# Kernel optimization log

Measured on AMD Instinct MI355X. Metric: run time of the kernel, lower is better.

Reference implementation:

```python
import jax, jax.numpy as jnp
import numpy as np

BN_EPS = 1e-5


def euclid_fc(x, w):
    """-1/2 * ||x_b - w_:,j||^2 for each (batch b, output j).
    x: [B, in], w: [in, out] -> [B, out].
    Uses the algebraic identity ||x-w||^2 = ||x||^2 - 2 x.w + ||w||^2,
    mathematically identical to the broadcast subtract-square-sum.
    """
    x_sq = jnp.sum(x * x, axis=-1, keepdims=True)      # [B, 1]
    w_sq = jnp.sum(w * w, axis=0)                       # [out]
    xw = x @ w                                          # [B, out]
    return -0.5 * (x_sq - 2.0 * xw + w_sq)


def batchnorm_train(x, gamma, beta):
    # BatchNorm1d in training mode: batch mean, biased variance, eps=1e-5
    mean = jnp.mean(x, axis=0)
    var = jnp.var(x, axis=0)  # biased, matches torch normalization stats
    return gamma * (x - mean) / jnp.sqrt(var + BN_EPS) + beta


def setup_inputs() -> dict:
    key = jax.random.key(0)
    ks = jax.random.split(key, 6)
    B, N_in, N2, N_bot, N_out = 1024, 784, 392, 8, 784
    X = jax.random.uniform(ks[0], (B, N_in), dtype=jnp.float32)
    W1 = jax.random.normal(ks[1], (N_in, N2), dtype=jnp.float32)
    W2 = jax.random.normal(ks[2], (N2, N_bot), dtype=jnp.float32)
    W3 = jax.random.normal(ks[3], (N_bot, N2), dtype=jnp.float32)
    W4 = jax.random.normal(ks[4], (N2, N_out), dtype=jnp.float32)
    return {
        "X": X,
        "W1": W1, "g1": jnp.ones((N2,), jnp.float32), "b1": jnp.zeros((N2,), jnp.float32),
        "W2": W2, "g2": jnp.ones((N_bot,), jnp.float32), "b2": jnp.zeros((N_bot,), jnp.float32),
        "W3": W3, "g3": jnp.ones((N2,), jnp.float32), "b3": jnp.zeros((N2,), jnp.float32),
        "W4": W4, "g4": jnp.ones((N_out,), jnp.float32), "b4": jnp.zeros((N_out,), jnp.float32),
    }


def reference(X, W1, g1, b1, W2, g2, b2, W3, g3, b3, W4, g4, b4):
    h = jax.nn.relu(batchnorm_train(euclid_fc(X, W1), g1, b1))
    h = jax.nn.relu(batchnorm_train(euclid_fc(h, W2), g2, b2))
    h = jax.nn.relu(batchnorm_train(euclid_fc(h, W3), g3, b3))
    out = jax.nn.sigmoid(batchnorm_train(euclid_fc(h, W4), g4, b4))
    return out
```

## Files before the change

kernel.cpp:

```cpp
#include <hip/hip_runtime.h>
#include <hip/hip_bf16.h>
#include <math.h>

#define BATCH 1024
#define BM 64
#define BN 64
#define BK 64
#define LDK 72
#define NRB 16

typedef __attribute__((ext_vector_type(8))) short bf16x8;
typedef __attribute__((ext_vector_type(8))) ushort ushort8;
typedef __attribute__((ext_vector_type(4))) float f32x4;

static __device__ __forceinline__ ushort f2bf(float f) {
    union { float f; unsigned u; } v; v.f = f;
    unsigned r = (v.u + 0x7fffu + ((v.u >> 16) & 1u)) >> 16;
    return (ushort)r;
}
static __device__ __forceinline__ float bf2f(ushort u) {
    union { unsigned u; float f; } v; v.u = ((unsigned)u) << 16;
    return v.f;
}

struct GemmSh {
    ushort As[2][BM][LDK];
    ushort Bs[2][BN][LDK];
    float bred[4 * BN];
    float xsq_s[BM], wsq_s[BN];
    float cs[2][BN], cq[2][BN];
};
struct Sh {
    union { float ptile[64][65]; GemmSh g; } u;
    float scaleK[784], shiftK[784];
};

static __device__ __forceinline__ void finalize_stats(
    const float2* __restrict__ stats_in, const float* __restrict__ gamma,
    const float* __restrict__ beta, int K, Sh& sh, int tid)
{
    for (int k = tid; k < K; k += 256) {
        const f32x4* p4 = (const f32x4*)(stats_in + (size_t)k * NRB);
        double s = 0.0, q = 0.0;
        #pragma unroll
        for (int i = 0; i < NRB / 2; ++i) {
            f32x4 v = p4[i];
            s += (double)v[0]; q += (double)v[1];
            s += (double)v[2]; q += (double)v[3];
        }
        double mean = s * (1.0 / BATCH);
        double var = q * (1.0 / BATCH) - mean * mean;
        float inv = (float)(1.0 / sqrt(var + 1e-5));
        float sc = gamma[k] * inv;
        sh.scaleK[k] = sc;
        sh.shiftK[k] = beta[k] - (float)mean * sc;
    }
    __syncthreads();
}

template <int NORM, int BSRC>
static __device__ void gemm_body(
    const float* __restrict__ A, const float* __restrict__ Bw32, const ushort* __restrict__ Wt,
    const float2* __restrict__ stats_in, const float* __restrict__ gamma, const float* __restrict__ beta,
    float* __restrict__ Z, float2* __restrict__ stats_out,
    int K, int N, int cx, int rb, Sh& sh, int tid)
{
    GemmSh& G = sh.u.g;
    const int lane = tid & 63;
    const int wv = tid >> 6;
    const int wr = wv >> 1, wc = wv & 1;
    const int row0 = rb * BM, col0 = cx * BN;
    const int ar = tid >> 3;
    const int ak0 = (tid & 7) * 8;
    const int bn = tid & 63;
    const int bk0 = (tid >> 6) * 16;
    const int fr = lane & 15;
    const int fg = lane >> 4;

    if (NORM) finalize_stats(stats_in, gamma, beta, K, sh, tid);

    f32x4 acc[2][2] = {};
    float asq[2] = {0.f, 0.f};
    float bsq = 0.f;
    float areg[2][8];
    float breg[16];
    ushort8 bh[2];
    const int ntiles = (K + BK - 1) / BK;

    auto load_tile = [&](int t) {
        const int kbase = t * BK;
        const int gc = col0 + bn;
        if (kbase + BK <= K) {
            #pragma unroll
            for (int l = 0; l < 2; ++l) {
                const float* p = A + (size_t)(row0 + ar + 32 * l) * K + kbase + ak0;
                f32x4 v0 = *(const f32x4*)p;
                f32x4 v1 = *(const f32x4*)(p + 4);
                #pragma unroll
                for (int j = 0; j < 4; ++j) { areg[l][j] = v0[j]; areg[l][4 + j] = v1[j]; }
                if (NORM) {
                    #pragma unroll
                    for (int j = 0; j < 8; ++j)
                        areg[l][j] = fmaxf(areg[l][j] * sh.scaleK[kbase + ak0 + j] + sh.shiftK[kbase + ak0 + j], 0.f);
                }
            }
            if (BSRC == 0) {
                #pragma unroll
                for (int i = 0; i < 16; ++i)
                    breg[i] = (gc < N) ? Bw32[(size_t)(kbase + bk0 + i) * N + gc] : 0.f;
            } else {
                if (gc < N) {
                    const ushort* q = Wt + (size_t)gc * K + kbase + bk0;
                    bh[0] = *(const ushort8*)q;
                    bh[1] = *(const ushort8*)(q + 8);
                } else {
                    bh[0] = (ushort8)0; bh[1] = (ushort8)0;
                }
            }
        } else {
            #pragma unroll
            for (int l = 0; l < 2; ++l)
                #pragma unroll
                for (int j = 0; j < 8; ++j) {
                    int gk = kbase + ak0 + j;
                    float x = 0.f;
                    if (gk < K) {
                        x = A[(size_t)(row0 + ar + 32 * l) * K + gk];
                        if (NORM) x = fmaxf(x * sh.scaleK[gk] + sh.shiftK[gk], 0.f);
                    }
                    areg[l][j] = x;
                }
            if (BSRC == 0) {
                #pragma unroll
                for (int i = 0; i < 16; ++i) {
                    int gk = kbase + bk0 + i;
                    breg[i] = (gk < K && gc < N) ? Bw32[(size_t)gk * N + gc] : 0.f;
                }
            } else {
                #pragma unroll
                for (int i = 0; i < 16; ++i) {
                    int gk = kbase + bk0 + i;
                    ushort u = (gk < K && gc < N) ? Wt[(size_t)gc * K + gk] : (ushort)0;
                    bh[i >> 3][i & 7] = u;
                }
            }
        }
    };

    auto store_tile = [&](int buf) {
        #pragma unroll
        for (int l = 0; l < 2; ++l) {
            ushort8 h;
            #pragma unroll
            for (int j = 0; j < 8; ++j) {
                h[j] = f2bf(areg[l][j]);
                asq[l] += areg[l][j] * areg[l][j];
            }
            *(ushort8*)&G.As[buf][ar + 32 * l][ak0] = h;
        }
        if (BSRC == 0) {
            ushort8 e0, e1;
            #pragma unroll
            for (int i = 0; i < 8; ++i) {
                e0[i] = f2bf(breg[i]);      bsq += breg[i] * breg[i];
                e1[i] = f2bf(breg[8 + i]);  bsq += breg[8 + i] * breg[8 + i];
            }
            *(ushort8*)&G.Bs[buf][bn][bk0] = e0;
            *(ushort8*)&G.Bs[buf][bn][bk0 + 8] = e1;
        } else {
            #pragma unroll
            for (int i = 0; i < 8; ++i) {
                float f0 = bf2f(bh[0][i]); bsq += f0 * f0;
                float f1 = bf2f(bh[1][i]); bsq += f1 * f1;
            }
            *(ushort8*)&G.Bs[buf][bn][bk0] = bh[0];
            *(ushort8*)&G.Bs[buf][bn][bk0 + 8] = bh[1];
        }
    };

    auto compute = [&](int buf) {
        bf16x8 af[2][2], bfr[2][2];
        #pragma unroll
        for (int m = 0; m < 2; ++m)
            #pragma unroll
            for (int kk = 0; kk < 2; ++kk)
                af[m][kk] = *(const bf16x8*)&G.As[buf][wr * 32 + m * 16 + fr][kk * 32 + fg * 8];
        #pragma unroll
        for (int n = 0; n < 2; ++n)
            #pragma unroll
            for (int kk = 0; kk < 2; ++kk)
                bfr[n][kk] = *(const bf16x8*)&G.Bs[buf][wc * 32 + n * 16 + fr][kk * 32 + fg * 8];
        #pragma unroll
        for (int m = 0; m < 2; ++m)
            #pragma unroll
            for (int n = 0; n < 2; ++n)
                #pragma unroll
                for (int kk = 0; kk < 2; ++kk)
                    acc[m][n] = __builtin_amdgcn_mfma_f32_16x16x32_bf16(af[m][kk], bfr[n][kk], acc[m][n], 0, 0, 0);
    };

    load_tile(0);
    store_tile(0);
    __syncthreads();
    for (int t = 0; t < ntiles; ++t) {
        if (t + 1 < ntiles) load_tile(t + 1);
        compute(t & 1);
        if (t + 1 < ntiles) store_tile((t + 1) & 1);
        __syncthreads();
    }

    #pragma unroll
    for (int l = 0; l < 2; ++l) {
        float s = asq[l];
        s += __shfl_xor(s, 1, 64);
        s += __shfl_xor(s, 2, 64);
        s += __shfl_xor(s, 4, 64);
        if ((tid & 7) == 0) G.xsq_s[ar + 32 * l] = s;
    }
    G.bred[(tid >> 6) * BN + bn] = bsq;
    __syncthreads();
    if (tid < BN) G.wsq_s[tid] = G.bred[0*BN+tid] + G.bred[1*BN+tid] + G.bred[2*BN+tid] + G.bred[3*BN+tid];
    __syncthreads();

    #pragma unroll
    for (int n = 0; n < 2; ++n) {
        const int c64 = wc * 32 + n * 16 + fr;
        const int c = col0 + c64;
        const float wsq = G.wsq_s[c64];
        float ps = 0.f, pq = 0.f;
        #pragma unroll
        for (int m = 0; m < 2; ++m) {
            #pragma unroll
            for (int j = 0; j < 4; ++j) {
                const int rl = wr * 32 + m * 16 + fg * 4 + j;
                float zv = acc[m][n][j] - 0.5f * (G.xsq_s[rl] + wsq);
                ps += zv; pq += zv * zv;
                if (c < N) Z[(size_t)(row0 + rl) * N + c] = zv;
            }
        }
        ps += __shfl_xor(ps, 16, 64); ps += __shfl_xor(ps, 32, 64);
        pq += __shfl_xor(pq, 16, 64); pq += __shfl_xor(pq, 32, 64);
        if (fg == 0) { G.cs[wr][c64] = ps; G.cq[wr][c64] = pq; }
    }
    __syncthreads();
    if (tid < BN) {
        int c = col0 + tid;
        if (c < N)
            stats_out[(size_t)c * NRB + rb] = make_float2(G.cs[0][tid] + G.cs[1][tid],
                                                          G.cq[0][tid] + G.cq[1][tid]);
    }
}

__global__ __launch_bounds__(256) void l1_kernel(
    const float* __restrict__ X, const float* __restrict__ W1,
    const float* __restrict__ W2, const float* __restrict__ W3, const float* __restrict__ W4,
    ushort* __restrict__ Wt2, ushort* __restrict__ Wt3, ushort* __restrict__ Wt4,
    float* __restrict__ z1, float2* __restrict__ st1)
{
    __shared__ Sh sh;
    const int tid = threadIdx.x;
    const int bid = blockIdx.x;

    if (bid < 112) {
        gemm_body<0, 0>(X, W1, nullptr, nullptr, nullptr, nullptr,
                        z1, st1, 784, 392, bid / 16, bid % 16, sh, tid);
        return;
    }
    for (int t = bid - 112; t < 105; t += 32) {
        const float* W; ushort* Wt; int K, N, kt, nt;
        if (t < 7)       { W = W2; Wt = Wt2; K = 392; N = 8;   kt = t;     nt = 0; }
        else if (t < 14) { W = W3; Wt = Wt3; K = 8;   N = 392; kt = 0;     nt = t - 7; }
        else             { int r = t - 14; W = W4; Wt = Wt4; K = 392; N = 784; kt = r % 7; nt = r / 7; }
        const int k0 = kt * 64, n0 = nt * 64;
        #pragma unroll
        for (int it = 0; it < 16; ++it) {
            int e = it * 256 + tid;
            int kk = e >> 6, nn = e & 63;
            int gk = k0 + kk, gn = n0 + nn;
            sh.u.ptile[kk][nn] = (gk < K && gn < N) ? W[(size_t)gk * N + gn] : 0.f;
        }
        __syncthreads();
        #pragma unroll
        for (int it = 0; it < 16; ++it) {
            int e = it * 256 + tid;
            int nn = e >> 6, kk = e & 63;
            int gk = k0 + kk, gn = n0 + nn;
            if (gk < K && gn < N) Wt[(size_t)gn * K + gk] = f2bf(sh.u.ptile[kk][nn]);
        }
        __syncthreads();
    }
}

__global__ __launch_bounds__(256) void gemm_norm_kernel(
    const float* __restrict__ A, const ushort* __restrict__ Wt,
    const float2* __restrict__ stats_in, const float* __restrict__ gamma, const float* __restrict__ beta,
    float* __restrict__ Z, float2* __restrict__ stats_out, int K, int N)
{
    __shared__ Sh sh;
    gemm_body<1, 1>(A, nullptr, Wt, stats_in, gamma, beta, Z, stats_out,
                    K, N, blockIdx.x / 16, blockIdx.x % 16, sh, threadIdx.x);
}

__global__ __launch_bounds__(256) void bn_sigmoid_inplace(
    float* __restrict__ Zout, const float2* __restrict__ stats,
    const float* __restrict__ gamma, const float* __restrict__ beta)
{
    const int N = 784;
    const int c0 = blockIdx.x * 16;
    const int r0 = blockIdx.y * 128;
    const int tid = threadIdx.x;
    __shared__ float sc16[16], sh16[16];

    if (tid < 16) {
        int k = c0 + tid;
        const f32x4* p4 = (const f32x4*)(stats + (size_t)k * NRB);
        double s = 0.0, q = 0.0;
        #pragma unroll
        for (int i = 0; i < NRB / 2; ++i) {
            f32x4 v = p4[i];
            s += (double)v[0]; q += (double)v[1];
            s += (double)v[2]; q += (double)v[3];
        }
        double mean = s * (1.0 / BATCH);
        double var = q * (1.0 / BATCH) - mean * mean;
        float inv = (float)(1.0 / sqrt(var + 1e-5));
        float scv = gamma[k] * inv;
        sc16[tid] = scv;
        sh16[tid] = beta[k] - (float)mean * scv;
    }
    __syncthreads();

    const int row = r0 + (tid & 127);
    const int ch = tid >> 7;
    float* p = Zout + (size_t)row * N + c0 + ch * 8;
    f32x4 v0 = *(f32x4*)p;
    f32x4 v1 = *(f32x4*)(p + 4);
    #pragma unroll
    for (int j = 0; j < 4; ++j) {
        float y0 = v0[j] * sc16[ch * 8 + j] + sh16[ch * 8 + j];
        v0[j] = 1.f / (1.f + expf(-y0));
        float y1 = v1[j] * sc16[ch * 8 + 4 + j] + sh16[ch * 8 + 4 + j];
        v1[j] = 1.f / (1.f + expf(-y1));
    }
    *(f32x4*)p = v0;
    *(f32x4*)(p + 4) = v1;
}

extern "C" void kernel_launch(void* const* d_in, const int* in_sizes, int n_in,
                              void* d_out, int out_size, void* d_ws, size_t ws_size,
                              hipStream_t stream) {
    const float* X  = (const float*)d_in[0];
    const float* W1 = (const float*)d_in[1];
    const float* g1 = (const float*)d_in[2];
    const float* b1 = (const float*)d_in[3];
    const float* W2 = (const float*)d_in[4];
    const float* g2 = (const float*)d_in[5];
    const float* b2 = (const float*)d_in[6];
    const float* W3 = (const float*)d_in[7];
    const float* g3 = (const float*)d_in[8];
    const float* b3 = (const float*)d_in[9];
    const float* W4 = (const float*)d_in[10];
    const float* g4 = (const float*)d_in[11];
    const float* b4 = (const float*)d_in[12];

    float* ws = (float*)d_ws;
    float*  z1  = ws;
    float*  z2  = z1 + 1024 * 392;
    float*  z3  = z2 + 1024 * 8;
    float2* st1 = (float2*)(z3 + 1024 * 392);
    float2* st2 = st1 + 392 * NRB;
    float2* st3 = st2 + 8 * NRB;
    float2* st4 = st3 + 392 * NRB;
    ushort* Wt2 = (ushort*)(st4 + 784 * NRB);
    ushort* Wt3 = Wt2 + 8 * 392;
    ushort* Wt4 = Wt3 + 392 * 8;
    float* outp = (float*)d_out;

    l1_kernel<<<144, 256, 0, stream>>>(X, W1, W2, W3, W4, Wt2, Wt3, Wt4, z1, st1);
    gemm_norm_kernel<<<16, 256, 0, stream>>>(z1, Wt2, st1, g1, b1, z2, st2, 392, 8);
    gemm_norm_kernel<<<112, 256, 0, stream>>>(z2, Wt3, st2, g2, b2, z3, st3, 8, 392);
    gemm_norm_kernel<<<208, 256, 0, stream>>>(z3, Wt4, st3, g3, b3, outp, st4, 392, 784);
    bn_sigmoid_inplace<<<dim3(49, 8), 256, 0, stream>>>(outp, st4, g4, b4);
}
```

Before: 67.29 us.

## Fuse layers 1-3 into one cooperative kernel with atomic flag gating

Merges the layer-1 GEMM, W4 transpose, layer-2 GEMM and the layer-3 FC/BN into a single cooperative launch. Dependent blocks spin on global atomic counters instead of waiting at kernel boundaries. Layer 3 (K=8) is now computed directly in registers with per-block full-batch BN statistics and writes a bf16 activation for layer 4, which reads bf16 A directly. The goal is to remove three kernel launches and the intermediate fp32 traffic, at the cost of spin-wait blocks, redundant BN2 statistics in each layer-3 block, and an added memset.

```diff
diff --git a/kernel.cpp b/kernel.cpp
--- a/kernel.cpp
+++ b/kernel.cpp
@@ -35,6 +35,20 @@
     float scaleK[784], shiftK[784];
 };
 
+static __device__ __forceinline__ void gate_signal(unsigned* f) {
+    __threadfence();
+    __syncthreads();
+    if (threadIdx.x == 0)
+        __hip_atomic_fetch_add(f, 1u, __ATOMIC_RELAXED, __HIP_MEMORY_SCOPE_AGENT);
+}
+static __device__ __forceinline__ void gate_wait(const unsigned* f, unsigned tgt) {
+    if (threadIdx.x == 0)
+        while (__hip_atomic_load(f, __ATOMIC_RELAXED, __HIP_MEMORY_SCOPE_AGENT) < tgt)
+            __builtin_amdgcn_s_sleep(2);
+    __syncthreads();
+    __threadfence();
+}
+
 static __device__ __forceinline__ void finalize_stats(
     const float2* __restrict__ stats_in, const float* __restrict__ gamma,
     const float* __restrict__ beta, int K, Sh& sh, int tid)
@@ -58,9 +72,10 @@
     __syncthreads();
 }
 
-template <int NORM, int BSRC>
+template <int NORM, int BSRC, int ASRC, int STATS>
 static __device__ void gemm_body(
-    const float* __restrict__ A, const float* __restrict__ Bw32, const ushort* __restrict__ Wt,
+    const float* __restrict__ A32, const ushort* __restrict__ A16,
+    const float* __restrict__ Bw32, const ushort* __restrict__ Wt,
     const float2* __restrict__ stats_in, const float* __restrict__ gamma, const float* __restrict__ beta,
     float* __restrict__ Z, float2* __restrict__ stats_out,
     int K, int N, int cx, int rb, Sh& sh, int tid)
@@ -83,6 +98,7 @@
     float asq[2] = {0.f, 0.f};
     float bsq = 0.f;
     float areg[2][8];
+    ushort8 ah[2];
     float breg[16];
     ushort8 bh[2];
     const int ntiles = (K + BK - 1) / BK;
@@ -93,15 +109,19 @@
         if (kbase + BK <= K) {
             #pragma unroll
             for (int l = 0; l < 2; ++l) {
-                const float* p = A + (size_t)(row0 + ar + 32 * l) * K + kbase + ak0;
-                f32x4 v0 = *(const f32x4*)p;
-                f32x4 v1 = *(const f32x4*)(p + 4);
-                #pragma unroll
-                for (int j = 0; j < 4; ++j) { areg[l][j] = v0[j]; areg[l][4 + j] = v1[j]; }
-                if (NORM) {
+                if (ASRC == 0) {
+                    const float* p = A32 + (size_t)(row0 + ar + 32 * l) * K + kbase + ak0;
+                    f32x4 v0 = *(const f32x4*)p;
+                    f32x4 v1 = *(const f32x4*)(p + 4);
                     #pragma unroll
-                    for (int j = 0; j < 8; ++j)
-                        areg[l][j] = fmaxf(areg[l][j] * sh.scaleK[kbase + ak0 + j] + sh.shiftK[kbase + ak0 + j], 0.f);
+                    for (int j = 0; j < 4; ++j) { areg[l][j] = v0[j]; areg[l][4 + j] = v1[j]; }
+                    if (NORM) {
+                        #pragma unroll
+                        for (int j = 0; j < 8; ++j)
+                            areg[l][j] = fmaxf(areg[l][j] * sh.scaleK[kbase + ak0 + j] + sh.shiftK[kbase + ak0 + j], 0.f);
+                    }
+                } else {
+                    ah[l] = *(const ushort8*)(A16 + (size_t)(row0 + ar + 32 * l) * K + kbase + ak0);
                 }
             }
             if (BSRC == 0) {
@@ -123,12 +143,16 @@
                 #pragma unroll
                 for (int j = 0; j < 8; ++j) {
                     int gk = kbase + ak0 + j;
-                    float x = 0.f;
-                    if (gk < K) {
-                        x = A[(size_t)(row0 + ar + 32 * l) * K + gk];
-                        if (NORM) x = fmaxf(x * sh.scaleK[gk] + sh.shiftK[gk], 0.f);
+                    if (ASRC == 0) {
+                        float x = 0.f;
+                        if (gk < K) {
+                            x = A32[(size_t)(row0 + ar + 32 * l) * K + gk];
+                            if (NORM) x = fmaxf(x * sh.scaleK[gk] + sh.shiftK[gk], 0.f);
+                        }
+                        areg[l][j] = x;
+                    } else {
+                        ah[l][j] = (gk < K) ? A16[(size_t)(row0 + ar + 32 * l) * K + gk] : (ushort)0;
                     }
-                    areg[l][j] = x;
                 }
             if (BSRC == 0) {
                 #pragma unroll
@@ -140,8 +164,7 @@
                 #pragma unroll
                 for (int i = 0; i < 16; ++i) {
                     int gk = kbase + bk0 + i;
-                    ushort u = (gk < K && gc < N) ? Wt[(size_t)gc * K + gk] : (ushort)0;
-                    bh[i >> 3][i & 7] = u;
+                    bh[i >> 3][i & 7] = (gk < K && gc < N) ? Wt[(size_t)gc * K + gk] : (ushort)0;
                 }
             }
         }
@@ -150,13 +173,22 @@
     auto store_tile = [&](int buf) {
         #pragma unroll
         for (int l = 0; l < 2; ++l) {
-            ushort8 h;
-            #pragma unroll
-            for (int j = 0; j < 8; ++j) {
-                h[j] = f2bf(areg[l][j]);
-                asq[l] += areg[l][j] * areg[l][j];
-            }
-            *(ushort8*)&G.As[buf][ar + 32 * l][ak0] = h;
+            if (ASRC == 0) {
+                ushort8 h;
+                #pragma unroll
+                for (int j = 0; j < 8; ++j) {
+                    h[j] = f2bf(areg[l][j]);
+                    asq[l] += areg[l][j] * areg[l][j];
+                }
+                *(ushort8*)&G.As[buf][ar + 32 * l][ak0] = h;
+            } else {
+                #pragma unroll
+                for (int j = 0; j < 8; ++j) {
+                    float x = bf2f(ah[l][j]);
+                    asq[l] += x * x;
+                }
+                *(ushort8*)&G.As[buf][ar + 32 * l][ak0] = ah[l];
+            }
         }
         if (BSRC == 0) {
             ushort8 e0, e1;
@@ -234,71 +266,188 @@
             for (int j = 0; j < 4; ++j) {
                 const int rl = wr * 32 + m * 16 + fg * 4 + j;
                 float zv = acc[m][n][j] - 0.5f * (G.xsq_s[rl] + wsq);
-                ps += zv; pq += zv * zv;
+                if (STATS) { ps += zv; pq += zv * zv; }
                 if (c < N) Z[(size_t)(row0 + rl) * N + c] = zv;
             }
         }
-        ps += __shfl_xor(ps, 16, 64); ps += __shfl_xor(ps, 32, 64);
-        pq += __shfl_xor(pq, 16, 64); pq += __shfl_xor(pq, 32, 64);
-        if (fg == 0) { G.cs[wr][c64] = ps; G.cq[wr][c64] = pq; }
-    }
-    __syncthreads();
-    if (tid < BN) {
-        int c = col0 + tid;
-        if (c < N)
-            stats_out[(size_t)c * NRB + rb] = make_float2(G.cs[0][tid] + G.cs[1][tid],
-                                                          G.cq[0][tid] + G.cq[1][tid]);
-    }
-}
-
-__global__ __launch_bounds__(256) void l1_kernel(
-    const float* __restrict__ X, const float* __restrict__ W1,
-    const float* __restrict__ W2, const float* __restrict__ W3, const float* __restrict__ W4,
-    ushort* __restrict__ Wt2, ushort* __restrict__ Wt3, ushort* __restrict__ Wt4,
-    float* __restrict__ z1, float2* __restrict__ st1)
+        if (STATS) {
+            ps += __shfl_xor(ps, 16, 64); ps += __shfl_xor(ps, 32, 64);
+            pq += __shfl_xor(pq, 16, 64); pq += __shfl_xor(pq, 32, 64);
+            if (fg == 0) { G.cs[wr][c64] = ps; G.cq[wr][c64] = pq; }
+        }
+    }
+    if (STATS) {
+        __syncthreads();
+        if (tid < BN) {
+            int c = col0 + tid;
+            if (c < N)
+                stats_out[(size_t)c * NRB + rb] = make_float2(G.cs[0][tid] + G.cs[1][tid],
+                                                              G.cq[0][tid] + G.cq[1][tid]);
+        }
+    }
+}
+
+static __device__ void l3fc_phase(
+    const float* __restrict__ z2, const float* __restrict__ W3,
+    const float* __restrict__ g2, const float* __restrict__ b2,
+    const float* __restrict__ g3, const float* __restrict__ b3,
+    ushort* __restrict__ h3, int sb, int tid, Sh& sh)
+{
+    float* S = sh.scaleK;
+    const int c0 = sb * 8;
+
+    if (tid < 64) S[tid] = W3[(tid >> 3) * 392 + c0 + (tid & 7)];
+    __syncthreads();
+    if (tid < 8) {
+        float q = 0.f;
+        #pragma unroll
+        for (int k = 0; k < 8; ++k) { float w = S[k * 8 + tid]; q += w * w; }
+        S[64 + tid] = q;
+    }
+
+    float z[4][8];
+    #pragma unroll
+    for (int i = 0; i < 4; ++i) {
+        const float* p = z2 + (size_t)(tid + i * 256) * 8;
+        f32x4 a = *(const f32x4*)p, b = *(const f32x4*)(p + 4);
+        #pragma unroll
+        for (int j = 0; j < 4; ++j) { z[i][j] = a[j]; z[i][4 + j] = b[j]; }
+    }
+
+    auto blk_red8 = [&](float v[8], int outoff, float scale) {
+        #pragma unroll
+        for (int m = 1; m < 64; m <<= 1)
+            #pragma unroll
+            for (int c = 0; c < 8; ++c) v[c] += __shfl_xor(v[c], m, 64);
+        if ((tid & 63) == 0) {
+            #pragma unroll
+            for (int c = 0; c < 8; ++c) sh.shiftK[(tid >> 6) * 8 + c] = v[c];
+        }
+        __syncthreads();
+        if (tid < 8) S[outoff + tid] =
+            (sh.shiftK[tid] + sh.shiftK[8 + tid] + sh.shiftK[16 + tid] + sh.shiftK[24 + tid]) * scale;
+        __syncthreads();
+    };
+
+    float s8[8];
+    #pragma unroll
+    for (int c = 0; c < 8; ++c) s8[c] = z[0][c] + z[1][c] + z[2][c] + z[3][c];
+    blk_red8(s8, 72, 1.f / BATCH);
+    #pragma unroll
+    for (int c = 0; c < 8; ++c) {
+        float q = 0.f;
+        #pragma unroll
+        for (int i = 0; i < 4; ++i) { float d = z[i][c] - S[72 + c]; q += d * d; }
+        s8[c] = q;
+    }
+    blk_red8(s8, 80, 1.f / BATCH);
+    if (tid < 8) {
+        float inv = 1.f / sqrtf(S[80 + tid] + 1e-5f);
+        float sc = g2[tid] * inv;
+        S[80 + tid] = sc;
+        S[88 + tid] = b2[tid] - S[72 + tid] * sc;
+    }
+    __syncthreads();
+
+    float h[4][8], z3v[4][8];
+    #pragma unroll
+    for (int i = 0; i < 4; ++i) {
+        float hs = 0.f;
+        #pragma unroll
+        for (int c = 0; c < 8; ++c) {
+            float x = fmaxf(z[i][c] * S[80 + c] + S[88 + c], 0.f);
+            h[i][c] = x; hs += x * x;
+        }
+        #pragma unroll
+        for (int c = 0; c < 8; ++c) {
+            float o = 0.f;
+            #pragma unroll
+            for (int k = 0; k < 8; ++k) o += h[i][k] * S[k * 8 + c];
+            z3v[i][c] = o - 0.5f * (hs + S[64 + c]);
+        }
+    }
+
+    #pragma unroll
+    for (int c = 0; c < 8; ++c) s8[c] = z3v[0][c] + z3v[1][c] + z3v[2][c] + z3v[3][c];
+    blk_red8(s8, 96, 1.f / BATCH);
+    #pragma unroll
+    for (int c = 0; c < 8; ++c) {
+        float q = 0.f;
+        #pragma unroll
+        for (int i = 0; i < 4; ++i) { float d = z3v[i][c] - S[96 + c]; q += d * d; }
+        s8[c] = q;
+    }
+    blk_red8(s8, 104, 1.f / BATCH);
+    if (tid < 8) {
+        float inv = 1.f / sqrtf(S[104 + tid] + 1e-5f);
+        float sc = g3[c0 + tid] * inv;
+        S[104 + tid] = sc;
+        S[112 + tid] = b3[c0 + tid] - S[96 + tid] * sc;
+    }
+    __syncthreads();
+    #pragma unroll
+    for (int i = 0; i < 4; ++i) {
+        ushort8 u;
+        #pragma unroll
+        for (int c = 0; c < 8; ++c)
+            u[c] = f2bf(fmaxf(z3v[i][c] * S[104 + c] + S[112 + c], 0.f));
+        *(ushort8*)&h3[(size_t)(tid + i * 256) * 392 + c0] = u;
+    }
+}
+
+__global__ __launch_bounds__(256) void k1_kernel(
+    const float* X, const float* W1, const float* g1, const float* b1,
+    const float* W2, const float* g2, const float* b2,
+    const float* W3, const float* g3, const float* b3,
+    const float* W4,
+    float* z1, float* z2, float2* st1, ushort* h3, ushort* Wt4, unsigned* flags)
 {
     __shared__ Sh sh;
-    const int tid = threadIdx.x;
-    const int bid = blockIdx.x;
+    const int tid = threadIdx.x, bid = blockIdx.x;
 
     if (bid < 112) {
-        gemm_body<0, 0>(X, W1, nullptr, nullptr, nullptr, nullptr,
-                        z1, st1, 784, 392, bid / 16, bid % 16, sh, tid);
-        return;
-    }
-    for (int t = bid - 112; t < 105; t += 32) {
-        const float* W; ushort* Wt; int K, N, kt, nt;
-        if (t < 7)       { W = W2; Wt = Wt2; K = 392; N = 8;   kt = t;     nt = 0; }
-        else if (t < 14) { W = W3; Wt = Wt3; K = 8;   N = 392; kt = 0;     nt = t - 7; }
-        else             { int r = t - 14; W = W4; Wt = Wt4; K = 392; N = 784; kt = r % 7; nt = r / 7; }
-        const int k0 = kt * 64, n0 = nt * 64;
-        #pragma unroll
-        for (int it = 0; it < 16; ++it) {
-            int e = it * 256 + tid;
-            int kk = e >> 6, nn = e & 63;
-            int gk = k0 + kk, gn = n0 + nn;
-            sh.u.ptile[kk][nn] = (gk < K && gn < N) ? W[(size_t)gk * N + gn] : 0.f;
-        }
-        __syncthreads();
-        #pragma unroll
-        for (int it = 0; it < 16; ++it) {
-            int e = it * 256 + tid;
-            int nn = e >> 6, kk = e & 63;
-            int gk = k0 + kk, gn = n0 + nn;
-            if (gk < K && gn < N) Wt[(size_t)gn * K + gk] = f2bf(sh.u.ptile[kk][nn]);
-        }
-        __syncthreads();
-    }
-}
-
-__global__ __launch_bounds__(256) void gemm_norm_kernel(
-    const float* __restrict__ A, const ushort* __restrict__ Wt,
-    const float2* __restrict__ stats_in, const float* __restrict__ gamma, const float* __restrict__ beta,
-    float* __restrict__ Z, float2* __restrict__ stats_out, int K, int N)
+        gemm_body<0, 0, 0, 1>(X, nullptr, W1, nullptr, nullptr, nullptr, nullptr,
+                              z1, st1, 784, 392, bid / 16, bid % 16, sh, tid);
+        gate_signal(&flags[0]);
+    } else if (bid < 144) {
+        for (int t = bid - 112; t < 91; t += 32) {
+            int kt = t % 7, nt = t / 7;
+            const int k0 = kt * 64, n0 = nt * 64;
+            #pragma unroll
+            for (int it = 0; it < 16; ++it) {
+                int e = it * 256 + tid;
+                int kk = e >> 6, nn = e & 63;
+                int gk = k0 + kk, gn = n0 + nn;
+                sh.u.ptile[kk][nn] = (gk < 392 && gn < 784) ? W4[(size_t)gk * 784 + gn] : 0.f;
+            }
+            __syncthreads();
+            #pragma unroll
+            for (int it = 0; it < 16; ++it) {
+                int e = it * 256 + tid;
+                int nn = e >> 6, kk = e & 63;
+                int gk = k0 + kk, gn = n0 + nn;
+                if (gk < 392 && gn < 784) Wt4[(size_t)gn * 392 + gk] = f2bf(sh.u.ptile[kk][nn]);
+            }
+            __syncthreads();
+        }
+    } else if (bid < 160) {
+        gate_wait(&flags[0], 112);
+        gemm_body<1, 0, 0, 0>(z1, nullptr, W2, nullptr, st1, g1, b1,
+                              z2, nullptr, 392, 8, 0, bid - 144, sh, tid);
+        gate_signal(&flags[1]);
+    } else if (bid < 209) {
+        gate_wait(&flags[1], 16);
+        l3fc_phase(z2, W3, g2, b2, g3, b3, h3, bid - 160, tid, sh);
+    }
+}
+
+__global__ __launch_bounds__(256) void l4_kernel(
+    const ushort* __restrict__ h3, const ushort* __restrict__ Wt4,
+    float* __restrict__ z4, float2* __restrict__ st4)
 {
     __shared__ Sh sh;
-    gemm_body<1, 1>(A, nullptr, Wt, stats_in, gamma, beta, Z, stats_out,
-                    K, N, blockIdx.x / 16, blockIdx.x % 16, sh, threadIdx.x);
+    gemm_body<0, 1, 1, 1>(nullptr, h3, nullptr, Wt4, nullptr, nullptr, nullptr,
+                          z4, st4, 392, 784, blockIdx.x / 16, blockIdx.x % 16, sh, threadIdx.x);
 }
 
 __global__ __launch_bounds__(256) void bn_sigmoid_inplace(
@@ -366,19 +515,25 @@
     float* ws = (float*)d_ws;
     float*  z1  = ws;
     float*  z2  = z1 + 1024 * 392;
-    float*  z3  = z2 + 1024 * 8;
-    float2* st1 = (float2*)(z3 + 1024 * 392);
-    float2* st2 = st1 + 392 * NRB;
-    float2* st3 = st2 + 8 * NRB;
-    float2* st4 = st3 + 392 * NRB;
-    ushort* Wt2 = (ushort*)(st4 + 784 * NRB);
-    ushort* Wt3 = Wt2 + 8 * 392;
-    ushort* Wt4 = Wt3 + 392 * 8;
+    float2* st1 = (float2*)(z2 + 1024 * 8);
+    float2* st4 = st1 + 392 * NRB;
+    ushort* h3  = (ushort*)(st4 + 784 * NRB);
+    ushort* Wt4 = h3 + 1024 * 392;
+    size_t flag_off = ((((char*)(Wt4 + 784 * 392)) - (char*)d_ws) + 255) & ~(size_t)255;
+    unsigned* flags = (unsigned*)((char*)d_ws + flag_off);
     float* outp = (float*)d_out;
 
-    l1_kernel<<<144, 256, 0, stream>>>(X, W1, W2, W3, W4, Wt2, Wt3, Wt4, z1, st1);
-    gemm_norm_kernel<<<16, 256, 0, stream>>>(z1, Wt2, st1, g1, b1, z2, st2, 392, 8);
-    gemm_norm_kernel<<<112, 256, 0, stream>>>(z2, Wt3, st2, g2, b2, z3, st3, 8, 392);
-    gemm_norm_kernel<<<208, 256, 0, stream>>>(z3, Wt4, st3, g3, b3, outp, st4, 392, 784);
+    hipMemsetAsync(flags, 0, 256, stream);
+
+    void* args[] = {
+        (void*)&X, (void*)&W1, (void*)&g1, (void*)&b1,
+        (void*)&W2, (void*)&g2, (void*)&b2,
+        (void*)&W3, (void*)&g3, (void*)&b3,
+        (void*)&W4,
+        (void*)&z1, (void*)&z2, (void*)&st1, (void*)&h3, (void*)&Wt4, (void*)&flags,
+    };
+    hipLaunchCooperativeKernel((void*)k1_kernel, dim3(209), dim3(256), args, 0, stream);
+
+    l4_kernel<<<208, 256, 0, stream>>>(h3, Wt4, outp, st4);
     bn_sigmoid_inplace<<<dim3(49, 8), 256, 0, stream>>>(outp, st4, g4, b4);
 }
```

New measurement: 102.7 us. +52.6%, slower.
